# Kernel tuning notes

Hardware: AMD Instinct MI355X
Metric: run time of the kernel (lower is better)

Reference implementation:

```python
import jax, jax.numpy as jnp
import numpy as np

N_FFT = 1024
HOP = 256
F_BINS = N_FFT // 2 + 1  # 513


def _make_dft_kernel():
    # torch.hann_window(N) is periodic: 0.5*(1 - cos(2*pi*k/N))
    window = 0.5 * (1.0 - np.cos(2.0 * np.pi * np.arange(N_FFT) / N_FFT))
    # rfft of identity, transposed -> (F, n_fft), then apply window along time axis
    dftm = np.fft.rfft(np.eye(N_FFT)).T * window[None, :]  # complex (F, n_fft)
    # view_as_real + rearrange 'f n ri -> (ri f) n': real block first, imag block second
    kernel = np.concatenate([dftm.real, dftm.imag], axis=0)  # (2F, n_fft)
    return jnp.asarray(kernel, dtype=jnp.float32)


def setup_inputs() -> dict:
    key = jax.random.key(0)
    signal = jax.random.normal(key, (16, 262144), dtype=jnp.float32)
    kernel = _make_dft_kernel()  # (1026, 1024) fixed windowed-DFT matrix (buffer)
    return {"signal": signal, "kernel": kernel}


def reference(signal, kernel):
    # center=True: reflect-pad by n_fft//2 on both sides
    pad = N_FFT // 2
    x = jnp.pad(signal, ((0, 0), (pad, pad)), mode="reflect")  # (B, L)
    B, L = x.shape
    n_frames = (L - N_FFT) // HOP + 1
    # im2col framing: (n_frames, n_fft) gather indices
    idx = jnp.arange(n_frames)[:, None] * HOP + jnp.arange(N_FFT)[None, :]
    frames = x[:, idx]  # (B, n_frames, n_fft)
    # conv1d as GEMM: (B, 2F, n_frames)
    out = jnp.einsum("btn,cn->bct", frames, kernel)
    # rearrange '(ri f) n -> f n ri' with ri outer
    out = out.reshape(B, 2, F_BINS, n_frames)
    return jnp.transpose(out, (0, 2, 3, 1))  # (B, F, n_frames, 2)
```

## Files before the change

### kernel.cpp

```cpp
#include <hip/hip_runtime.h>
#include <hip/hip_bf16.h>
#include <cstdint>


#define HOP 256
#define NFFT 1024
#define FB 513
#define NT 1025
#define NBATCH 16
#define MCH 1026
#define MP2 1280
#define SIGLEN 262144
#define SIGP 263168
#define BM 256
#define BN 128
#define BK 64
#define NKT 16
#define SLOT_BYTES 49152
#define LDS_BYTES (3 * SLOT_BYTES)

typedef __attribute__((ext_vector_type(8))) short short8;
typedef __attribute__((ext_vector_type(4))) float f32x4;
typedef unsigned int u32;

__device__ __forceinline__ unsigned short f2bf(float f) {
  u32 u = __float_as_uint(f);
  u = (u + 0x7FFFu + ((u >> 16) & 1u)) >> 16;
  return (unsigned short)u;
}
__device__ __forceinline__ float bf2f(unsigned short s) {
  return __uint_as_float(((u32)s) << 16);
}

__global__ __launch_bounds__(256) void prep_A(const float* __restrict__ kern,
                                              unsigned short* __restrict__ A) {
  size_t i8 = ((size_t)blockIdx.x * 256 + threadIdx.x) * 8;
  int row = (int)(i8 >> 10);
  int col = (int)(i8 & 1023);
  short8 v = {0, 0, 0, 0, 0, 0, 0, 0};
  if (row < MCH) {
    int f = row >> 1, ri = row & 1;
    int src_row = ri * FB + f;
    const float* s = kern + ((size_t)src_row << 10) + col;
#pragma unroll
    for (int e = 0; e < 8; ++e) v[e] = (short)f2bf(s[e]);
  }
  *(short8*)(A + i8) = v;
}

__global__ __launch_bounds__(256) void prep_S(const float* __restrict__ sig,
                                              unsigned short* __restrict__ S) {
  size_t i8 = ((size_t)blockIdx.x * 256 + threadIdx.x) * 8;
  int b = (int)(i8 / SIGP);
  int i = (int)(i8 - (size_t)b * SIGP);
  const float* sb = sig + (size_t)b * SIGLEN;
  short8 v;
#pragma unroll
  for (int e = 0; e < 8; ++e) {
    int j = i + e - 512;
    j = (j < 0) ? -j : j;
    j = (j >= SIGLEN) ? (2 * SIGLEN - 2 - j) : j;
    v[e] = (short)f2bf(sb[j]);
  }
  *(short8*)(S + i8) = v;
}

__device__ __forceinline__ void async16(void* lds, const void* g) {
  __builtin_amdgcn_global_load_lds(
      (const __attribute__((address_space(1))) u32*)g,
      (__attribute__((address_space(3))) u32*)lds, 16, 0, 0);
}

__global__ __launch_bounds__(512, 2) void stft_mm(const unsigned short* __restrict__ A,
                                                  const unsigned short* __restrict__ S,
                                                  float* __restrict__ out) {
  extern __shared__ char smem[];

  const int tid = threadIdx.x;
  const int lane = tid & 63;
  const int wid = tid >> 6;
  const int wr = wid >> 1;
  const int wc = wid & 1;
  const int lr = lane & 15;
  const int g16 = lane >> 4;

  const int bid = blockIdx.x;
  const int wg = (bid & 7) * 64 + (bid >> 3);
  const int mt = wg & 3;
  const int r2 = wg >> 2;
  const int nt = r2 & 7;
  const int b  = r2 >> 3;

  const int c0 = mt * BM;
  const int t0 = nt * BN;

  const char* Ab = (const char*)A;
  const char* Sb = (const char*)(S + (size_t)b * SIGP);

#define STAGE_TILE(kt, s)                                                      \
  {                                                                            \
    char* As_ = smem + (s) * SLOT_BYTES;                                       \
    char* Bs_ = As_ + 32768;                                                   \
    _Pragma("unroll") for (int j = 0; j < 4; ++j) {                            \
      const int G0 = j * 512 + wid * 64;                                       \
      u32 p = (u32)(G0 + lane) * 16u;                                          \
      u32 q = p ^ (((p >> 7) & 7u) << 4);                                      \
      const char* src = Ab + ((size_t)(c0 + (int)(q >> 7)) << 11)              \
                           + (kt) * 128 + (int)(q & 127u);                     \
      async16(As_ + (size_t)G0 * 16u, src);                                    \
    }                                                                          \
    _Pragma("unroll") for (int j = 0; j < 2; ++j) {                            \
      const int G0 = j * 512 + wid * 64;                                       \
      u32 p = (u32)(G0 + lane) * 16u;                                          \
      u32 q = p ^ (((p >> 7) & 7u) << 4);                                      \
      const char* src = Sb + ((size_t)(t0 + (int)(q >> 7)) << 9)               \
                           + (kt) * 128 + (int)(q & 127u);                     \
      async16(Bs_ + (size_t)G0 * 16u, src);                                    \
    }                                                                          \
  }

  STAGE_TILE(0, 0)
  STAGE_TILE(1, 1)
  asm volatile("s_waitcnt vmcnt(6)" ::: "memory");
  __builtin_amdgcn_s_barrier();
  asm volatile("" ::: "memory");

  u32 qa[4], qb[4];
#pragma unroll
  for (int mi = 0; mi < 4; ++mi) qa[mi] = (u32)((wr * 64 + mi * 16 + lr) * 128 + g16 * 16);
#pragma unroll
  for (int ni = 0; ni < 4; ++ni) qb[ni] = (u32)((wc * 64 + ni * 16 + lr) * 128 + g16 * 16);

  f32x4 acc[4][4] = {};

#pragma unroll
  for (int k = 0; k < NKT; ++k) {
    const char* As = smem + (k % 3) * SLOT_BYTES;
    const char* Bs = As + 32768;
    short8 af[2][4], bfv[2][4];
#pragma unroll
    for (int h = 0; h < 2; ++h) {
#pragma unroll
      for (int mi = 0; mi < 4; ++mi) {
        u32 q = qa[mi] + (u32)(h * 64);
        u32 p = q ^ (((q >> 7) & 7u) << 4);
        af[h][mi] = *(const short8*)(As + p);
      }
#pragma unroll
      for (int ni = 0; ni < 4; ++ni) {
        u32 q = qb[ni] + (u32)(h * 64);
        u32 p = q ^ (((q >> 7) & 7u) << 4);
        bfv[h][ni] = *(const short8*)(Bs + p);
      }
    }
    if (k + 2 < NKT) STAGE_TILE(k + 2, (k + 2) % 3)
#pragma unroll
    for (int h = 0; h < 2; ++h)
#pragma unroll
      for (int mi = 0; mi < 4; ++mi)
#pragma unroll
        for (int ni = 0; ni < 4; ++ni)
          acc[mi][ni] = __builtin_amdgcn_mfma_f32_16x16x32_bf16(
              af[h][mi], bfv[h][ni], acc[mi][ni], 0, 0, 0);
    if (k <= NKT - 3)      asm volatile("s_waitcnt vmcnt(6)" ::: "memory");
    else                   asm volatile("s_waitcnt vmcnt(0)" ::: "memory");
    __builtin_amdgcn_s_barrier();
    asm volatile("" ::: "memory");
  }
#undef STAGE_TILE

#pragma unroll
  for (int mi = 0; mi < 4; ++mi) {
    const int cb = c0 + wr * 64 + mi * 16 + g16 * 4;
    const int f0 = cb >> 1;
#pragma unroll
    for (int ni = 0; ni < 4; ++ni) {
      const int t = t0 + wc * 64 + ni * 16 + lr;
      *(float2*)(out + ((((size_t)b * FB + f0) * NT + t) << 1)) =
          make_float2(acc[mi][ni][0], acc[mi][ni][1]);
      *(float2*)(out + ((((size_t)b * FB + f0 + 1) * NT + t) << 1)) =
          make_float2(acc[mi][ni][2], acc[mi][ni][3]);
    }
  }
}

__global__ __launch_bounds__(256) void stft_edge(const unsigned short* __restrict__ A,
                                                 const unsigned short* __restrict__ S,
                                                 float* __restrict__ out) {
  const int wv = blockIdx.x * 4 + (threadIdx.x >> 6);
  const int lane = threadIdx.x & 63;
  int b, f, t;
  if (wv < NBATCH * NT) {
    b = wv / NT; t = wv - b * NT; f = FB - 1;
  } else {
    int u = wv - NBATCH * NT;
    b = u / FB; f = u - b * FB; t = NT - 1;
  }
  const unsigned short* w  = S + (size_t)b * SIGP + (size_t)t * HOP + lane * 16;
  const unsigned short* r0 = A + ((size_t)(2 * f) << 10) + lane * 16;
  const unsigned short* r1 = r0 + 1024;
  short8 wv0 = *(const short8*)w,  wv1 = *(const short8*)(w + 8);
  short8 a0  = *(const short8*)r0, a1  = *(const short8*)(r0 + 8);
  short8 b0  = *(const short8*)r1, b1  = *(const short8*)(r1 + 8);
  float d0 = 0.f, d1 = 0.f;
#pragma unroll
  for (int e = 0; e < 8; ++e) {
    float x0 = bf2f((unsigned short)wv0[e]), x1 = bf2f((unsigned short)wv1[e]);
    d0 += bf2f((unsigned short)a0[e]) * x0 + bf2f((unsigned short)a1[e]) * x1;
    d1 += bf2f((unsigned short)b0[e]) * x0 + bf2f((unsigned short)b1[e]) * x1;
  }
#pragma unroll
  for (int m = 32; m; m >>= 1) {
    d0 += __shfl_xor(d0, m);
    d1 += __shfl_xor(d1, m);
  }
  if (lane == 0)
    *(float2*)(out + ((((size_t)b * FB + f) * NT + t) << 1)) = make_float2(d0, d1);
}

extern "C" void kernel_launch(void* const* d_in, const int* in_sizes, int n_in,
                              void* d_out, int out_size, void* d_ws, size_t ws_size,
                              hipStream_t stream) {
  const float* sig = (const float*)d_in[0];
  const float* kern = (const float*)d_in[1];
  float* out = (float*)d_out;

  unsigned short* wsA = (unsigned short*)d_ws;
  unsigned short* wsS = wsA + (size_t)MP2 * NFFT;

  (void)hipFuncSetAttribute((const void*)stft_mm,
                            hipFuncAttributeMaxDynamicSharedMemorySize, LDS_BYTES);

  prep_A<<<dim3(MP2 * NFFT / 8 / 256), 256, 0, stream>>>(kern, wsA);
  prep_S<<<dim3(NBATCH * SIGP / 8 / 256), 256, 0, stream>>>(sig, wsS);
  stft_mm<<<dim3(4 * 8 * NBATCH), 512, LDS_BYTES, stream>>>(wsA, wsS, out);
  stft_edge<<<dim3((NBATCH * NT + NBATCH * FB) / 4), 256, 0, stream>>>(wsA, wsS, out);
}
```

Before: 64.97 us.

## Split K-tile into two half-phases with interleaved staging, barriers and setprio

Splits each BK=64 iteration into two sub-phases. Each phase issues half of the LDS fragment reads and half of the next tile's async global-to-LDS loads, then runs 16 MFMAs under raised wave priority (s_setprio). Extra barriers bracket each MFMA cluster so waves stay aligned, in the style of ping-pong scheduling. It aims to interleave memory issue with matrix compute and cut register pressure from holding both fragment halves. In exchange it adds four barriers per iteration, which can cost sync overhead.

```diff
diff --git a/kernel.cpp b/kernel.cpp
--- a/kernel.cpp
+++ b/kernel.cpp
@@ -97,30 +97,30 @@
   const char* Ab = (const char*)A;
   const char* Sb = (const char*)(S + (size_t)b * SIGP);
 
-#define STAGE_TILE(kt, s)                                                      \
+#define STAGE_PART(kt, s, j)                                                   \
   {                                                                            \
     char* As_ = smem + (s) * SLOT_BYTES;                                       \
-    char* Bs_ = As_ + 32768;                                                   \
-    _Pragma("unroll") for (int j = 0; j < 4; ++j) {                            \
-      const int G0 = j * 512 + wid * 64;                                       \
+    if ((j) < 4) {                                                             \
+      const int G0 = (j) * 512 + wid * 64;                                     \
       u32 p = (u32)(G0 + lane) * 16u;                                          \
       u32 q = p ^ (((p >> 7) & 7u) << 4);                                      \
       const char* src = Ab + ((size_t)(c0 + (int)(q >> 7)) << 11)              \
                            + (kt) * 128 + (int)(q & 127u);                     \
       async16(As_ + (size_t)G0 * 16u, src);                                    \
-    }                                                                          \
-    _Pragma("unroll") for (int j = 0; j < 2; ++j) {                            \
-      const int G0 = j * 512 + wid * 64;                                       \
+    } else {                                                                   \
+      const int G0 = ((j) - 4) * 512 + wid * 64;                               \
       u32 p = (u32)(G0 + lane) * 16u;                                          \
       u32 q = p ^ (((p >> 7) & 7u) << 4);                                      \
       const char* src = Sb + ((size_t)(t0 + (int)(q >> 7)) << 9)               \
                            + (kt) * 128 + (int)(q & 127u);                     \
-      async16(Bs_ + (size_t)G0 * 16u, src);                                    \
+      async16(As_ + 32768 + (size_t)G0 * 16u, src);                            \
     }                                                                          \
   }
 
-  STAGE_TILE(0, 0)
-  STAGE_TILE(1, 1)
+#pragma unroll
+  for (int j = 0; j < 6; ++j) STAGE_PART(0, 0, j)
+#pragma unroll
+  for (int j = 0; j < 6; ++j) STAGE_PART(1, 1, j)
   asm volatile("s_waitcnt vmcnt(6)" ::: "memory");
   __builtin_amdgcn_s_barrier();
   asm volatile("" ::: "memory");
@@ -137,37 +137,73 @@
   for (int k = 0; k < NKT; ++k) {
     const char* As = smem + (k % 3) * SLOT_BYTES;
     const char* Bs = As + 32768;
-    short8 af[2][4], bfv[2][4];
-#pragma unroll
-    for (int h = 0; h < 2; ++h) {
-#pragma unroll
-      for (int mi = 0; mi < 4; ++mi) {
-        u32 q = qa[mi] + (u32)(h * 64);
-        u32 p = q ^ (((q >> 7) & 7u) << 4);
-        af[h][mi] = *(const short8*)(As + p);
-      }
-#pragma unroll
-      for (int ni = 0; ni < 4; ++ni) {
-        u32 q = qb[ni] + (u32)(h * 64);
-        u32 p = q ^ (((q >> 7) & 7u) << 4);
-        bfv[h][ni] = *(const short8*)(Bs + p);
-      }
-    }
-    if (k + 2 < NKT) STAGE_TILE(k + 2, (k + 2) % 3)
-#pragma unroll
-    for (int h = 0; h < 2; ++h)
-#pragma unroll
-      for (int mi = 0; mi < 4; ++mi)
-#pragma unroll
-        for (int ni = 0; ni < 4; ++ni)
-          acc[mi][ni] = __builtin_amdgcn_mfma_f32_16x16x32_bf16(
-              af[h][mi], bfv[h][ni], acc[mi][ni], 0, 0, 0);
+    const int ks = (k + 2) % 3;
+
+    short8 af0[4], bf0[4];
+#pragma unroll
+    for (int mi = 0; mi < 4; ++mi) {
+      u32 q = qa[mi];
+      u32 p = q ^ (((q >> 7) & 7u) << 4);
+      af0[mi] = *(const short8*)(As + p);
+    }
+#pragma unroll
+    for (int ni = 0; ni < 4; ++ni) {
+      u32 q = qb[ni];
+      u32 p = q ^ (((q >> 7) & 7u) << 4);
+      bf0[ni] = *(const short8*)(Bs + p);
+    }
+    if (k + 2 < NKT) {
+      STAGE_PART(k + 2, ks, 0)
+      STAGE_PART(k + 2, ks, 1)
+      STAGE_PART(k + 2, ks, 2)
+    }
+    __builtin_amdgcn_s_barrier();
+    asm volatile("s_waitcnt lgkmcnt(0)" ::: "memory");
+    __builtin_amdgcn_s_setprio(1);
+#pragma unroll
+    for (int mi = 0; mi < 4; ++mi)
+#pragma unroll
+      for (int ni = 0; ni < 4; ++ni)
+        acc[mi][ni] = __builtin_amdgcn_mfma_f32_16x16x32_bf16(
+            af0[mi], bf0[ni], acc[mi][ni], 0, 0, 0);
+    __builtin_amdgcn_s_setprio(0);
+    __builtin_amdgcn_s_barrier();
+    asm volatile("" ::: "memory");
+
+    short8 af1[4], bf1[4];
+#pragma unroll
+    for (int mi = 0; mi < 4; ++mi) {
+      u32 q = qa[mi] + 64u;
+      u32 p = q ^ (((q >> 7) & 7u) << 4);
+      af1[mi] = *(const short8*)(As + p);
+    }
+#pragma unroll
+    for (int ni = 0; ni < 4; ++ni) {
+      u32 q = qb[ni] + 64u;
+      u32 p = q ^ (((q >> 7) & 7u) << 4);
+      bf1[ni] = *(const short8*)(Bs + p);
+    }
+    if (k + 2 < NKT) {
+      STAGE_PART(k + 2, ks, 3)
+      STAGE_PART(k + 2, ks, 4)
+      STAGE_PART(k + 2, ks, 5)
+    }
     if (k <= NKT - 3)      asm volatile("s_waitcnt vmcnt(6)" ::: "memory");
     else                   asm volatile("s_waitcnt vmcnt(0)" ::: "memory");
     __builtin_amdgcn_s_barrier();
+    asm volatile("s_waitcnt lgkmcnt(0)" ::: "memory");
+    __builtin_amdgcn_s_setprio(1);
+#pragma unroll
+    for (int mi = 0; mi < 4; ++mi)
+#pragma unroll
+      for (int ni = 0; ni < 4; ++ni)
+        acc[mi][ni] = __builtin_amdgcn_mfma_f32_16x16x32_bf16(
+            af1[mi], bf1[ni], acc[mi][ni], 0, 0, 0);
+    __builtin_amdgcn_s_setprio(0);
+    __builtin_amdgcn_s_barrier();
     asm volatile("" ::: "memory");
   }
-#undef STAGE_TILE
+#undef STAGE_PART
 
 #pragma unroll
   for (int mi = 0; mi < 4; ++mi) {
```

Result: slower. 67.44 us (+3.8%).

## Stage contiguous signal window in LDS once and double-buffer kernel tiles

Applied to the files above, without the earlier changes.

Overlapping STFT frames are no longer staged as separate B tiles per K step. Each block now loads the whole contiguous bf16 signal window its 128 frames cover into LDS once, with a row-XOR swizzle, and indexes frames directly from it. This removes redundant global and LDS fill traffic for the B operand. The DFT-matrix tiles go from a triple-buffered to a double-buffered pipeline synchronized by __syncthreads. The larger LDS footprint drops occupancy to one block per CU, so the 512-block grid runs in more waves, and the pipeline prefetches only one step ahead.

```diff
diff --git a/kernel.cpp b/kernel.cpp
--- a/kernel.cpp
+++ b/kernel.cpp
@@ -16,8 +16,10 @@
 #define BN 128
 #define BK 64
 #define NKT 16
-#define SLOT_BYTES 49152
-#define LDS_BYTES (3 * SLOT_BYTES)
+#define A_SLOT 32768
+#define WBYTES 67584
+#define WGRAN (WBYTES / 16)
+#define LDS_BYTES (2 * A_SLOT + WBYTES)
 
 typedef __attribute__((ext_vector_type(8))) short short8;
 typedef __attribute__((ext_vector_type(4))) float f32x4;
@@ -71,10 +73,11 @@
       (__attribute__((address_space(3))) u32*)lds, 16, 0, 0);
 }
 
-__global__ __launch_bounds__(512, 2) void stft_mm(const unsigned short* __restrict__ A,
+__global__ __launch_bounds__(512, 1) void stft_mm(const unsigned short* __restrict__ A,
                                                   const unsigned short* __restrict__ S,
                                                   float* __restrict__ out) {
   extern __shared__ char smem[];
+  char* const sWin = smem + 2 * A_SLOT;
 
   const int tid = threadIdx.x;
   const int lane = tid & 63;
@@ -95,12 +98,11 @@
   const int t0 = nt * BN;
 
   const char* Ab = (const char*)A;
-  const char* Sb = (const char*)(S + (size_t)b * SIGP);
-
-#define STAGE_TILE(kt, s)                                                      \
+  const char* Sb = (const char*)(S + (size_t)b * SIGP) + (size_t)nt * 65536;
+
+#define STAGE_A(kt, s)                                                         \
   {                                                                            \
-    char* As_ = smem + (s) * SLOT_BYTES;                                       \
-    char* Bs_ = As_ + 32768;                                                   \
+    char* As_ = smem + (s) * A_SLOT;                                           \
     _Pragma("unroll") for (int j = 0; j < 4; ++j) {                            \
       const int G0 = j * 512 + wid * 64;                                       \
       u32 p = (u32)(G0 + lane) * 16u;                                          \
@@ -109,34 +111,37 @@
                            + (kt) * 128 + (int)(q & 127u);                     \
       async16(As_ + (size_t)G0 * 16u, src);                                    \
     }                                                                          \
-    _Pragma("unroll") for (int j = 0; j < 2; ++j) {                            \
-      const int G0 = j * 512 + wid * 64;                                       \
-      u32 p = (u32)(G0 + lane) * 16u;                                          \
-      u32 q = p ^ (((p >> 7) & 7u) << 4);                                      \
-      const char* src = Sb + ((size_t)(t0 + (int)(q >> 7)) << 9)               \
-                           + (kt) * 128 + (int)(q & 127u);                     \
-      async16(Bs_ + (size_t)G0 * 16u, src);                                    \
-    }                                                                          \
-  }
-
-  STAGE_TILE(0, 0)
-  STAGE_TILE(1, 1)
-  asm volatile("s_waitcnt vmcnt(6)" ::: "memory");
-  __builtin_amdgcn_s_barrier();
-  asm volatile("" ::: "memory");
+  }
+
+#pragma unroll
+  for (int i = 0; i < 8; ++i) {
+    const int base = i * 512 + wid * 64;
+    u32 p = (u32)(base + lane) * 16u;
+    u32 q = p ^ (((p >> 9) & 7u) << 4);
+    async16(sWin + (size_t)base * 16u, Sb + q);
+  }
+  if (wid < 2) {
+    const int base = 4096 + wid * 64;
+    u32 p = (u32)(base + lane) * 16u;
+    u32 q = p ^ (((p >> 9) & 7u) << 4);
+    async16(sWin + (size_t)base * 16u, Sb + q);
+  }
+  STAGE_A(0, 0)
+  __syncthreads();
 
   u32 qa[4], qb[4];
 #pragma unroll
   for (int mi = 0; mi < 4; ++mi) qa[mi] = (u32)((wr * 64 + mi * 16 + lr) * 128 + g16 * 16);
 #pragma unroll
-  for (int ni = 0; ni < 4; ++ni) qb[ni] = (u32)((wc * 64 + ni * 16 + lr) * 128 + g16 * 16);
+  for (int ni = 0; ni < 4; ++ni) qb[ni] = (u32)((wc * 64 + ni * 16 + lr) * 512 + g16 * 16);
 
   f32x4 acc[4][4] = {};
 
 #pragma unroll
   for (int k = 0; k < NKT; ++k) {
-    const char* As = smem + (k % 3) * SLOT_BYTES;
-    const char* Bs = As + 32768;
+    const char* As = smem + (k & 1) * A_SLOT;
+    if (k + 1 < NKT) STAGE_A(k + 1, (k + 1) & 1)
+
     short8 af[2][4], bfv[2][4];
 #pragma unroll
     for (int h = 0; h < 2; ++h) {
@@ -148,12 +153,11 @@
       }
 #pragma unroll
       for (int ni = 0; ni < 4; ++ni) {
-        u32 q = qb[ni] + (u32)(h * 64);
-        u32 p = q ^ (((q >> 7) & 7u) << 4);
-        bfv[h][ni] = *(const short8*)(Bs + p);
+        u32 q = qb[ni] + (u32)(k * 128 + h * 64);
+        u32 p = q ^ (((q >> 9) & 7u) << 4);
+        bfv[h][ni] = *(const short8*)(sWin + p);
       }
     }
-    if (k + 2 < NKT) STAGE_TILE(k + 2, (k + 2) % 3)
 #pragma unroll
     for (int h = 0; h < 2; ++h)
 #pragma unroll
@@ -162,12 +166,10 @@
         for (int ni = 0; ni < 4; ++ni)
           acc[mi][ni] = __builtin_amdgcn_mfma_f32_16x16x32_bf16(
               af[h][mi], bfv[h][ni], acc[mi][ni], 0, 0, 0);
-    if (k <= NKT - 3)      asm volatile("s_waitcnt vmcnt(6)" ::: "memory");
-    else                   asm volatile("s_waitcnt vmcnt(0)" ::: "memory");
-    __builtin_amdgcn_s_barrier();
-    asm volatile("" ::: "memory");
-  }
-#undef STAGE_TILE
+
+    if (k + 1 < NKT) __syncthreads();
+  }
+#undef STAGE_A
 
 #pragma unroll
   for (int mi = 0; mi < 4; ++mi) {
```

Measured after the change: 66.05 us. Within noise of the previous version (+1.7%).

## Enlarge GEMM tile to 256x256 with BK=32 and k-group-major LDS layout

Applied to the files above, without the earlier changes.

The STFT GEMM kernel's N tile grows from 128 to 256 frames and its K step drops from 64 to 32, so each wave computes a 128x64 sub-tile with 8x4 MFMA accumulators. The LDS layout changes from an XOR-swizzled row-major layout to a k-group-major layout (16-byte chunks grouped by k offset), which removes the swizzle arithmetic. The grid halves to 256 workgroups, fewer than the CU count. In exchange it doubles accumulator registers, doubles the number of K iterations and barriers, and may add LDS bank conflicts.

```diff
diff --git a/kernel.cpp b/kernel.cpp
--- a/kernel.cpp
+++ b/kernel.cpp
@@ -13,10 +13,10 @@
 #define SIGLEN 262144
 #define SIGP 263168
 #define BM 256
-#define BN 128
-#define BK 64
-#define NKT 16
-#define SLOT_BYTES 49152
+#define BN 256
+#define BK 32
+#define NKT 32
+#define SLOT_BYTES 32768
 #define LDS_BYTES (3 * SLOT_BYTES)
 
 typedef __attribute__((ext_vector_type(8))) short short8;
@@ -79,17 +79,17 @@
   const int tid = threadIdx.x;
   const int lane = tid & 63;
   const int wid = tid >> 6;
-  const int wr = wid >> 1;
-  const int wc = wid & 1;
+  const int wr = wid >> 2;
+  const int wc = wid & 3;
   const int lr = lane & 15;
   const int g16 = lane >> 4;
 
   const int bid = blockIdx.x;
-  const int wg = (bid & 7) * 64 + (bid >> 3);
+  const int wg = (bid & 7) * 32 + (bid >> 3);
   const int mt = wg & 3;
   const int r2 = wg >> 2;
-  const int nt = r2 & 7;
-  const int b  = r2 >> 3;
+  const int nt = r2 & 3;
+  const int b  = r2 >> 2;
 
   const int c0 = mt * BM;
   const int t0 = nt * BN;
@@ -100,78 +100,69 @@
 #define STAGE_TILE(kt, s)                                                      \
   {                                                                            \
     char* As_ = smem + (s) * SLOT_BYTES;                                       \
-    char* Bs_ = As_ + 32768;                                                   \
-    _Pragma("unroll") for (int j = 0; j < 4; ++j) {                            \
+    char* Bs_ = As_ + 16384;                                                   \
+    _Pragma("unroll") for (int j = 0; j < 2; ++j) {                            \
       const int G0 = j * 512 + wid * 64;                                       \
-      u32 p = (u32)(G0 + lane) * 16u;                                          \
-      u32 q = p ^ (((p >> 7) & 7u) << 4);                                      \
-      const char* src = Ab + ((size_t)(c0 + (int)(q >> 7)) << 11)              \
-                           + (kt) * 128 + (int)(q & 127u);                     \
-      async16(As_ + (size_t)G0 * 16u, src);                                    \
+      const int G = G0 + lane;                                                 \
+      const int row = G & 255, g = G >> 8;                                     \
+      const char* srcA = Ab + ((size_t)(c0 + row) << 11) + (kt) * 64 + g * 16; \
+      async16(As_ + (size_t)G0 * 16u, srcA);                                   \
     }                                                                          \
     _Pragma("unroll") for (int j = 0; j < 2; ++j) {                            \
       const int G0 = j * 512 + wid * 64;                                       \
-      u32 p = (u32)(G0 + lane) * 16u;                                          \
-      u32 q = p ^ (((p >> 7) & 7u) << 4);                                      \
-      const char* src = Sb + ((size_t)(t0 + (int)(q >> 7)) << 9)               \
-                           + (kt) * 128 + (int)(q & 127u);                     \
-      async16(Bs_ + (size_t)G0 * 16u, src);                                    \
+      const int G = G0 + lane;                                                 \
+      const int row = G & 255, g = G >> 8;                                     \
+      const char* srcB = Sb + ((size_t)(t0 + row) << 9) + (kt) * 64 + g * 16;  \
+      async16(Bs_ + (size_t)G0 * 16u, srcB);                                   \
     }                                                                          \
   }
 
   STAGE_TILE(0, 0)
   STAGE_TILE(1, 1)
-  asm volatile("s_waitcnt vmcnt(6)" ::: "memory");
+  asm volatile("s_waitcnt vmcnt(4)" ::: "memory");
   __builtin_amdgcn_s_barrier();
   asm volatile("" ::: "memory");
 
-  u32 qa[4], qb[4];
-#pragma unroll
-  for (int mi = 0; mi < 4; ++mi) qa[mi] = (u32)((wr * 64 + mi * 16 + lr) * 128 + g16 * 16);
-#pragma unroll
-  for (int ni = 0; ni < 4; ++ni) qb[ni] = (u32)((wc * 64 + ni * 16 + lr) * 128 + g16 * 16);
-
-  f32x4 acc[4][4] = {};
+  u32 oa[8], ob[4];
+#pragma unroll
+  for (int mi = 0; mi < 8; ++mi) oa[mi] = (u32)(g16 * 4096 + (wr * 128 + mi * 16 + lr) * 16);
+#pragma unroll
+  for (int ni = 0; ni < 4; ++ni) ob[ni] = (u32)(g16 * 4096 + (wc * 64 + ni * 16 + lr) * 16);
+
+  f32x4 acc[8][4] = {};
 
 #pragma unroll
   for (int k = 0; k < NKT; ++k) {
     const char* As = smem + (k % 3) * SLOT_BYTES;
-    const char* Bs = As + 32768;
-    short8 af[2][4], bfv[2][4];
-#pragma unroll
-    for (int h = 0; h < 2; ++h) {
-#pragma unroll
-      for (int mi = 0; mi < 4; ++mi) {
-        u32 q = qa[mi] + (u32)(h * 64);
-        u32 p = q ^ (((q >> 7) & 7u) << 4);
-        af[h][mi] = *(const short8*)(As + p);
-      }
-#pragma unroll
-      for (int ni = 0; ni < 4; ++ni) {
-        u32 q = qb[ni] + (u32)(h * 64);
-        u32 p = q ^ (((q >> 7) & 7u) << 4);
-        bfv[h][ni] = *(const short8*)(Bs + p);
-      }
+    const char* Bs = As + 16384;
+
+    short8 af[8], bfv[4];
+#pragma unroll
+    for (int mi = 0; mi < 8; ++mi) af[mi] = *(const short8*)(As + oa[mi]);
+#pragma unroll
+    for (int ni = 0; ni < 4; ++ni) bfv[ni] = *(const short8*)(Bs + ob[ni]);
+
+    if (k + 2 < NKT) STAGE_TILE(k + 2, (k + 2) % 3)
+
+#pragma unroll
+    for (int mi = 0; mi < 8; ++mi)
+#pragma unroll
+      for (int ni = 0; ni < 4; ++ni)
+        acc[mi][ni] = __builtin_amdgcn_mfma_f32_16x16x32_bf16(
+            af[mi], bfv[ni], acc[mi][ni], 0, 0, 0);
+
+    if (k + 1 < NKT) {
+      if (k <= NKT - 3) asm volatile("s_waitcnt vmcnt(4)" ::: "memory");
+      else              asm volatile("s_waitcnt vmcnt(0)" ::: "memory");
+      __builtin_amdgcn_s_barrier();
+      asm volatile("" ::: "memory");
     }
-    if (k + 2 < NKT) STAGE_TILE(k + 2, (k + 2) % 3)
-#pragma unroll
-    for (int h = 0; h < 2; ++h)
-#pragma unroll
-      for (int mi = 0; mi < 4; ++mi)
-#pragma unroll
-        for (int ni = 0; ni < 4; ++ni)
-          acc[mi][ni] = __builtin_amdgcn_mfma_f32_16x16x32_bf16(
-              af[h][mi], bfv[h][ni], acc[mi][ni], 0, 0, 0);
-    if (k <= NKT - 3)      asm volatile("s_waitcnt vmcnt(6)" ::: "memory");
-    else                   asm volatile("s_waitcnt vmcnt(0)" ::: "memory");
-    __builtin_amdgcn_s_barrier();
-    asm volatile("" ::: "memory");
   }
 #undef STAGE_TILE
 
 #pragma unroll
-  for (int mi = 0; mi < 4; ++mi) {
-    const int cb = c0 + wr * 64 + mi * 16 + g16 * 4;
+  for (int mi = 0; mi < 8; ++mi) {
+    const int cb = c0 + wr * 128 + mi * 16 + g16 * 4;
     const int f0 = cb >> 1;
 #pragma unroll
     for (int ni = 0; ni < 4; ++ni) {
@@ -233,6 +224,6 @@
 
   prep_A<<<dim3(MP2 * NFFT / 8 / 256), 256, 0, stream>>>(kern, wsA);
   prep_S<<<dim3(NBATCH * SIGP / 8 / 256), 256, 0, stream>>>(sig, wsS);
-  stft_mm<<<dim3(4 * 8 * NBATCH), 512, LDS_BYTES, stream>>>(wsA, wsS, out);
+  stft_mm<<<dim3(4 * 4 * NBATCH), 512, LDS_BYTES, stream>>>(wsA, wsS, out);
   stft_edge<<<dim3((NBATCH * NT + NBATCH * FB) / 4), 256, 0, stream>>>(wsA, wsS, out);
 }
```

New measurement: 86.71 us. +33.5%, slower.
